# Optimization experiments

Measured on AMD Instinct MI355X. Metric: run time of the kernel, lower is better.

The kernel has to match this reference:

```python
import jax, jax.numpy as jnp
import numpy as np
from jax import lax


def _conv(x, w, b, pad, dil):
    # standard NCHW conv, OIHW weights
    y = lax.conv_general_dilated(x, w, (1, 1), [(pad, pad), (pad, pad)],
                                 rhs_dilation=(dil, dil),
                                 dimension_numbers=('NCHW', 'OIHW', 'NCHW'))
    return y + b[None, :, None, None]


def _bilinear(img, py, px):
    # img: [B,C,H,W]; py,px: [B,KK,H,W] float sample positions.
    # Zero-padding bilinear sampling (torchvision deform_conv semantics):
    # each of the 4 corners contributes 0 if it lies outside the image.
    B, C, H, W = img.shape
    y0 = jnp.floor(py)
    x0 = jnp.floor(px)
    wy1 = py - y0
    wx1 = px - x0
    imgf = img.reshape(B, C, H * W)

    def corner(yi, xi, wgt):
        valid = (yi >= 0) & (yi <= H - 1) & (xi >= 0) & (xi <= W - 1)
        yc = jnp.clip(yi, 0, H - 1).astype(jnp.int32)
        xc = jnp.clip(xi, 0, W - 1).astype(jnp.int32)
        idx = yc * W + xc  # [B,KK,H,W]
        g = jax.vmap(lambda im, ix: jnp.take(im, ix.reshape(-1), axis=1))(imgf, idx)
        g = g.reshape(B, C, *yi.shape[1:])  # [B,C,KK,H,W]
        return g * (wgt * valid.astype(img.dtype))[:, None]

    return (corner(y0, x0, (1 - wy1) * (1 - wx1))
            + corner(y0, x0 + 1, (1 - wy1) * wx1)
            + corner(y0 + 1, x0, wy1 * (1 - wx1))
            + corner(y0 + 1, x0 + 1, wy1 * wx1))


def _deform_dw(x, off_w, off_b, dw_w, K, pad, dil):
    # offset-predicted deformable depthwise conv (groups == channels)
    B, C, H, W = x.shape
    off = _conv(x, off_w, off_b, pad, dil).reshape(B, K * K, 2, H, W)
    dy, dx = off[:, :, 0], off[:, :, 1]  # torchvision order: (dy, dx) per tap
    ky, kx = jnp.meshgrid(jnp.arange(K), jnp.arange(K), indexing='ij')
    by = (ky.reshape(-1) * dil - pad).astype(x.dtype)  # [KK]
    bx = (kx.reshape(-1) * dil - pad).astype(x.dtype)
    py = jnp.arange(H, dtype=x.dtype)[None, None, :, None] + by[None, :, None, None] + dy
    px = jnp.arange(W, dtype=x.dtype)[None, None, None, :] + bx[None, :, None, None] + dx
    s = _bilinear(x, py, px)  # [B,C,KK,H,W]
    return jnp.einsum('bckhw,ck->bchw', s, dw_w.reshape(C, K * K))


def setup_inputs() -> dict:
    key = jax.random.key(0)
    ks = jax.random.split(key, 9)
    B, C, H, W = 4, 64, 56, 56
    f = lambda k, shape, s: jax.random.normal(k, shape, jnp.float32) * s
    return dict(
        x=f(ks[0], (B, C, H, W), 1.0),
        off_w1=f(ks[1], (2 * 5 * 5, C, 5, 5), 0.01), off_b1=f(ks[2], (2 * 5 * 5,), 0.01),
        dw_w1=f(ks[3], (C, 1, 5, 5), 0.1),
        off_w2=f(ks[4], (2 * 7 * 7, C, 7, 7), 0.01), off_b2=f(ks[5], (2 * 7 * 7,), 0.01),
        dw_w2=f(ks[6], (C, 1, 7, 7), 0.1),
        pw_w=f(ks[7], (C, C, 1, 1), 0.05), pw_b=f(ks[8], (C,), 0.05),
    )


def reference(x, off_w1, off_b1, dw_w1, off_w2, off_b2, dw_w2, pw_w, pw_b):
    attn = _deform_dw(x, off_w1, off_b1, dw_w1, 5, 2, 1)       # 5x5 deformable dw
    attn = _deform_dw(attn, off_w2, off_b2, dw_w2, 7, 9, 3)    # 7x7 dil-3 deformable dw
    attn = _conv(attn, pw_w, pw_b, 0, 1)                       # 1x1 pointwise
    return x * attn                                            # gated multiply
```

## Files before the change

kernel.cpp:

```cpp
#include <hip/hip_runtime.h>

#define BB 4
#define CC 64
#define HH 56
#define WW 56
#define HW (HH*WW)

typedef unsigned short u16;
typedef unsigned int u32;
typedef __attribute__((ext_vector_type(8))) short bf16x8;
typedef __attribute__((ext_vector_type(4))) float f32x4;

__device__ __forceinline__ u16 f2bf(float f) {
    union { float f; unsigned u; } c; c.f = f;
    unsigned u = c.u;
    u = (u + 0x7FFFu + ((u >> 16) & 1u)) >> 16;
    return (u16)u;
}
__device__ __forceinline__ float lo_f(u32 u) {
    union { unsigned u; float f; } c; c.u = u << 16; return c.f;
}
__device__ __forceinline__ float hi_f(u32 u) {
    union { unsigned u; float f; } c; c.u = u & 0xffff0000u; return c.f;
}

typedef const __attribute__((address_space(1))) unsigned int guint;
typedef __attribute__((address_space(3))) unsigned int luint;
__device__ __forceinline__ void gl_lds16(const void* g, void* l) {
    __builtin_amdgcn_global_load_lds((guint*)g, (luint*)l, 16, 0, 0);
}

#define W1P 60
#define PB1 3600
#define W2P 74
#define PB2 5476

#define R1 102400
#define R2 401408
#define R3 4096
#define R4 1600
#define R5 3136
#define R6z (BB*PB1*8)
#define R7z (BB*PB2*8)
#define TGRID (BB*(HW/64))
#define PREPN (R1+R2+R3+R4+R5+R6z+R7z)
__global__ __launch_bounds__(256)
void prep_tr_kernel(const float* __restrict__ x,
                    const float* __restrict__ ow1, const float* __restrict__ ow2,
                    const float* __restrict__ pw,  const float* __restrict__ dw1,
                    const float* __restrict__ dw2,
                    u16* __restrict__ xTp, u16* __restrict__ a1Tp,
                    u16* __restrict__ w2t1, u16* __restrict__ w2t2,
                    u16* __restrict__ pwT, float* __restrict__ dwT1,
                    float* __restrict__ dwT2) {
    __shared__ u16 tile[64][72];
    const int t = threadIdx.x;
    if (blockIdx.x < TGRID) {
        const int blk = blockIdx.x;
        const int b   = blk / (HW/64);
        const int p0  = (blk % (HW/64))*64;
        const int px  = t & 63, icq = t >> 6;
        const float* ip = x + ((size_t)b*CC + icq*16)*HW + p0 + px;
        #pragma unroll
        for (int i = 0; i < 16; ++i)
            tile[px][icq*16 + i] = f2bf(ip[(size_t)i*HW]);
        __syncthreads();
        const int px2 = t >> 2, g = t & 3;
        const int p = p0 + px2;
        const int y = p / WW, xw = p % WW;
        u16* op = xTp + ((size_t)b*PB1 + (y+2)*W1P + (xw+2))*64 + g*16;
        const uint4* s = (const uint4*)&tile[px2][g*16];
        ((uint4*)op)[0] = s[0];
        ((uint4*)op)[1] = s[1];
        return;
    }
    const int i = (blockIdx.x - TGRID)*256 + t;
    if (i < R1) {
        const int ic = i & 63, n = (i >> 6) & 63, tap = i >> 12;
        w2t1[i] = f2bf((n < 50) ? ow1[((size_t)n*64 + ic)*25 + tap] : 0.f);
    } else if (i < R1+R2) {
        const int j = i - R1;
        const int ic = j & 63, n = (j >> 6) & 127, tap = j >> 13;
        w2t2[j] = f2bf((n < 98) ? ow2[((size_t)n*64 + ic)*49 + tap] : 0.f);
    } else if (i < R1+R2+R3) {
        const int j = i - (R1+R2);
        pwT[j] = f2bf(pw[j]);
    } else if (i < R1+R2+R3+R4) {
        const int j = i - (R1+R2+R3);
        const int c = j & 63, k = j >> 6;
        dwT1[j] = dw1[c*25 + k];
    } else if (i < R1+R2+R3+R4+R5) {
        const int j = i - (R1+R2+R3+R4);
        const int c = j & 63, k = j >> 6;
        dwT2[j] = dw2[c*49 + k];
    } else if (i < R1+R2+R3+R4+R5+R6z) {
        const int j = i - (R1+R2+R3+R4+R5);
        const int c8 = j & 7, q = j >> 3;
        const int px = q % PB1, bz = q / PB1;
        const int y = px / W1P, xx = px % W1P;
        if (y < 2 || y >= 58 || xx < 2 || xx >= 58)
            *(uint4*)(xTp + ((size_t)bz*PB1 + px)*64 + c8*8) = make_uint4(0,0,0,0);
    } else if (i < PREPN) {
        const int j = i - (R1+R2+R3+R4+R5+R6z);
        const int c8 = j & 7, q = j >> 3;
        const int px = q % PB2, bz = q / PB2;
        const int y = px / W2P, xx = px % W2P;
        if (y < 9 || y >= 65 || xx < 9 || xx >= 65)
            *(uint4*)(a1Tp + ((size_t)bz*PB2 + px)*64 + c8*8) = make_uint4(0,0,0,0);
    }
}

template<int K, int DIL, int PAD, int COUT, int NP, int NPAD, int NTW>
__global__ __launch_bounds__(256, 4)
void conv_mfma_lds_kernel(const u16* __restrict__ xTp, const u16* __restrict__ w2t,
                          const float* __restrict__ bias, float* __restrict__ out) {
    constexpr int KK = K*K;
    constexpr int BROWS = 16*NTW;
    constexpr int WP  = WW + 2*PAD;
    constexpr int IPB = (HH + 2*PAD)*WP;
    __shared__ u16 Ab[2][64*64];
    __shared__ u16 Bb[2][BROWS*64];

    const int nm   = HW/64;
    const int b    = blockIdx.x / nm;
    const int p0   = (blockIdx.x % nm)*64;
    const int nt0  = blockIdx.y;
    const int t    = threadIdx.x;
    const int wave = t >> 6;
    const int lane = t & 63;

    const int spx = t >> 3;
    const int sc  = t & 7;
    const int gk8 = ((sc - spx) & 7)*8;
    const int pA  = p0 + spx;
    const int pB  = pA + 32;
    const int pyA = pA / WW, pxA = pA % WW;
    const int pyB = pB / WW, pxB = pB % WW;
    const u16* xb  = xTp + (size_t)b*IPB*64;
    const u16* gA0 = xb + ((size_t)((pyA+PAD)*WP + (pxA+PAD)))*64 + gk8;
    const u16* gA1 = xb + ((size_t)((pyB+PAD)*WP + (pxB+PAD)))*64 + gk8;
    const u16* gB  = w2t + (size_t)nt0*BROWS*64 + spx*64 + gk8;

    const int r = lane & 15, quad = lane >> 4;
    const int mloc = wave*16 + r;
    const int arow = mloc*64;
    const int a0s = ((quad     + mloc) & 7)*8;
    const int a1s = ((quad + 4 + mloc) & 7)*8;
    const int b0s = ((quad     + r) & 7)*8;
    const int b1s = ((quad + 4 + r) & 7)*8;

    f32x4 acc[NTW];
    #pragma unroll
    for (int h = 0; h < NTW; ++h) acc[h] = (f32x4){0.f,0.f,0.f,0.f};

    auto ISSUE = [&](int tap, int buf) {
        const int dyy = (tap/K)*DIL - PAD;
        const int dxx = (tap%K)*DIL - PAD;
        const int toff = (dyy*WP + dxx)*64;
        gl_lds16(gA0 + toff,           &Ab[buf][wave*512]);
        gl_lds16(gA1 + toff,           &Ab[buf][2048 + wave*512]);
        gl_lds16(gB + tap*(NP*64),     &Bb[buf][wave*512]);
    };

    ISSUE(0, 0);
    __syncthreads();

    #pragma unroll
    for (int tap = 0; tap < KK; ++tap) {
        if (tap + 1 < KK) ISSUE(tap + 1, (tap + 1) & 1);

        const u16* A  = &Ab[tap & 1][0];
        const u16* Bq = &Bb[tap & 1][0];
        const bf16x8 av0 = *(const bf16x8*)(A + arow + a0s);
        const bf16x8 av1 = *(const bf16x8*)(A + arow + a1s);
        #pragma unroll
        for (int h = 0; h < NTW; ++h) {
            const int brow = (h*16 + r)*64;
            const bf16x8 bv0 = *(const bf16x8*)(Bq + brow + b0s);
            const bf16x8 bv1 = *(const bf16x8*)(Bq + brow + b1s);
            acc[h] = __builtin_amdgcn_mfma_f32_16x16x32_bf16(av0, bv0, acc[h], 0, 0, 0);
            acc[h] = __builtin_amdgcn_mfma_f32_16x16x32_bf16(av1, bv1, acc[h], 0, 0, 0);
        }
        __syncthreads();
    }

    #pragma unroll
    for (int h = 0; h < NTW; ++h) {
        const int n = nt0*BROWS + h*16 + r;
        if (n < COUT) {
            const float bv = bias[n];
            float* op = out + ((size_t)b*HW + p0 + wave*16 + quad*4)*NPAD + n;
            #pragma unroll
            for (int r2 = 0; r2 < 4; ++r2) op[(size_t)r2*NPAD] = acc[h][r2] + bv;
        }
    }
}

template<int K, int DIL, int PAD, int NPAD,
         int IP, int IWP, int IPB, int OP, int OWP, int OPB>
__global__ __launch_bounds__(256)
void deform_cl_kernel(const u16* __restrict__ inT, const float* __restrict__ offT,
                      const float* __restrict__ dwT, u16* __restrict__ outT) {
    constexpr int KK = K*K;
    __shared__ float4 swt[8][KK];
    __shared__ int4   sat[8][KK];
    __shared__ float  sdw[KK*64];

    const int t = threadIdx.x;
    const int nb8 = (BB*HW/8) >> 3;
    const int blk0 = blockIdx.x;
    const int blk = (blk0 & 7)*nb8 + (blk0 >> 3);
    const int p0 = blk*8;
    const int b  = p0 / HW;
    const int pl0 = p0 - b*HW;

    for (int i = t; i < KK*64; i += 256) sdw[i] = dwT[i];

    for (int i = t; i < 8*KK; i += 256) {
        const int pix = i / KK, k = i - pix*KK;
        const int pl  = pl0 + pix;
        const int h = pl / WW, w = pl % WW;
        const float* orow = offT + ((size_t)b*HW + pl)*NPAD;
        const float dy = orow[2*k];
        const float dx = orow[2*k+1];
        const float py = (float)(h + (k/K)*DIL - PAD) + dy;
        const float px = (float)(w + (k%K)*DIL - PAD) + dx;
        const float y0f = floorf(py), x0f = floorf(px);
        const float wy1 = py - y0f,  wx1 = px - x0f;
        const float wy0 = 1.f - wy1, wx0 = 1.f - wx1;
        const int y0 = (int)y0f, x0 = (int)x0f;

        const int y0c = min(max(y0,   0), HH-1);
        const int y1c = min(max(y0+1, 0), HH-1);
        const int x0c = min(max(x0,   0), WW-1);
        const int x1c = min(max(x0+1, 0), WW-1);
        const float gy0 = wy0 * ((y0   >= 0 && y0   < HH) ? 1.f : 0.f);
        const float gy1 = wy1 * ((y0+1 >= 0 && y0+1 < HH) ? 1.f : 0.f);
        const float gx0 = wx0 * ((x0   >= 0 && x0   < WW) ? 1.f : 0.f);
        const float gx1 = wx1 * ((x0+1 >= 0 && x0+1 < WW) ? 1.f : 0.f);

        swt[pix][k] = make_float4(gy0*gx0, gy0*gx1, gy1*gx0, gy1*gx1);
        const int r0 = (y0c + IP)*IWP, r1 = (y1c + IP)*IWP;
        sat[pix][k] = make_int4((r0 + x0c + IP) << 7, (r0 + x1c + IP) << 7,
                                (r1 + x0c + IP) << 7, (r1 + x1c + IP) << 7);
    }
    __syncthreads();

    const int wave = t >> 6, lane = t & 63;
    const int pixl = 2*wave + (lane >> 5);
    const int chp  = lane & 31;
    const char* ib = (const char*)(inT + (size_t)b*IPB*64) + chp*4;

    float accx = 0.f, accy = 0.f;

    int4   av[3];
    float4 wv[2];
    float2 dv[2];
    u32 c00[2], c01[2], c10[2], c11[2];

    av[0] = sat[pixl][0];
    if (KK > 1) av[1] = sat[pixl][1];
    wv[0] = swt[pixl][0];
    dv[0] = *(const float2*)&sdw[2*chp];
    c00[0] = *(const u32*)(ib + av[0].x);
    c01[0] = *(const u32*)(ib + av[0].y);
    c10[0] = *(const u32*)(ib + av[0].z);
    c11[0] = *(const u32*)(ib + av[0].w);

    #pragma unroll
    for (int k = 0; k < KK; ++k) {
        const int kn = k + 1;
        if (kn + 1 < KK) av[(kn+1)%3] = sat[pixl][kn+1];
        if (kn < KK) {
            wv[kn&1] = swt[pixl][kn];
            dv[kn&1] = *(const float2*)&sdw[kn*64 + 2*chp];
            const int4 a = av[kn%3];
            c00[kn&1] = *(const u32*)(ib + a.x);
            c01[kn&1] = *(const u32*)(ib + a.y);
            c10[kn&1] = *(const u32*)(ib + a.z);
            c11[kn&1] = *(const u32*)(ib + a.w);
        }
        const float4 w = wv[k&1];
        const u32 u00 = c00[k&1], u01 = c01[k&1], u10 = c10[k&1], u11 = c11[k&1];
        const float sx = lo_f(u00)*w.x + lo_f(u01)*w.y + lo_f(u10)*w.z + lo_f(u11)*w.w;
        const float sy = hi_f(u00)*w.x + hi_f(u01)*w.y + hi_f(u10)*w.z + hi_f(u11)*w.w;
        const float2 d = dv[k&1];
        accx += sx * d.x;
        accy += sy * d.y;
    }

    const int oy = (pl0 + pixl) / WW, ox = (pl0 + pixl) % WW;
    const int opx = (oy + OP)*OWP + (ox + OP);
    const u32 o = (u32)f2bf(accx) | ((u32)f2bf(accy) << 16);
    *(u32*)((char*)outT + ((size_t)b*OPB + opx)*128 + chp*4) = o;
}

__global__ __launch_bounds__(256)
void pw_mfma_kernel(const u16* __restrict__ a2T, const u16* __restrict__ pwT,
                    const float* __restrict__ pb, const float* __restrict__ x,
                    float* __restrict__ out) {
    const int nm = HW/64;
    const int b  = blockIdx.x / nm;
    const int p0 = (blockIdx.x % nm)*64 + (threadIdx.x >> 6)*16;
    const int nt = blockIdx.y;
    const int lane = threadIdx.x & 63;
    const int r = lane & 15, quad = lane >> 4;

    const u16* ap = a2T + ((size_t)b*HW + p0 + r)*64 + quad*8;
    f32x4 acc = (f32x4){0.f,0.f,0.f,0.f};
    #pragma unroll
    for (int ks = 0; ks < 2; ++ks) {
        const bf16x8 av = *(const bf16x8*)(ap + ks*32);
        const bf16x8 bv = *(const bf16x8*)(pwT + ((size_t)(nt*16 + r))*64 + ks*32 + quad*8);
        acc = __builtin_amdgcn_mfma_f32_16x16x32_bf16(av, bv, acc, 0, 0, 0);
    }

    const int n = nt*16 + r;
    const float bv = pb[n];
    const size_t base = ((size_t)b*CC + n)*HW + p0 + quad*4;
    #pragma unroll
    for (int r2 = 0; r2 < 4; ++r2)
        out[base + r2] = x[base + r2] * (acc[r2] + bv);
}

template<int K, int DIL, int PAD, int COUT, int OCB>
__global__ __launch_bounds__(256)
void off_conv_sg_kernel(const float* __restrict__ in, const float* __restrict__ wgt,
                        const float* __restrict__ bias, float* __restrict__ out) {
    constexpr int KK = K*K;
    const int nOB = COUT / OCB;
    const int b   = blockIdx.x / nOB;
    const int oc0 = (blockIdx.x % nOB) * OCB;
    const int x   = threadIdx.x;
    const int h   = blockIdx.y*4 + threadIdx.y;

    float acc[OCB];
    #pragma unroll
    for (int o = 0; o < OCB; ++o) acc[o] = bias[oc0+o];

    const float* inb = in + (size_t)b*CC*HW;
    const float* wb  = wgt + (size_t)oc0*CC*KK;

    for (int ic = 0; ic < CC; ++ic) {
        const float* inp = inb + ic*HW;
        const float* wp  = wb + ic*KK;
        #pragma unroll
        for (int ky = 0; ky < K; ++ky) {
            const int  y  = h + ky*DIL - PAD;
            const bool yv = (y >= 0) && (y < HH);
            const int  yc = yv ? y : 0;
            const float* row = inp + yc*WW;
            #pragma unroll
            for (int kx = 0; kx < K; ++kx) {
                const int  xx = x + kx*DIL - PAD;
                const bool v  = yv && (xx >= 0) && (xx < WW);
                const int  xc = (xx < 0) ? 0 : ((xx >= WW) ? (WW-1) : xx);
                float val = row[xc];
                val = v ? val : 0.f;
                const int t = ky*K + kx;
                #pragma unroll
                for (int o = 0; o < OCB; ++o)
                    acc[o] += wp[(size_t)o*CC*KK + t] * val;
            }
        }
    }

    if (x >= WW) return;
    #pragma unroll
    for (int o = 0; o < OCB; ++o)
        out[((size_t)b*COUT + oc0 + o)*HW + h*WW + x] = acc[o];
}

template<int K, int DIL, int PAD>
__global__ __launch_bounds__(64)
void deform_dw_full_kernel(const float* __restrict__ in, const float* __restrict__ off,
                           const float* __restrict__ dw, float* __restrict__ out) {
    constexpr int KK = K*K;
    const int idx = blockIdx.x*64 + threadIdx.x;
    const int x = idx % WW;
    const int h = (idx / WW) % HH;
    const int c = (idx / HW) % CC;
    const int b = idx / (CC*HW);

    const float* inp  = in  + ((size_t)b*CC + c)*HW;
    const float* offp = off + (size_t)b*(2*KK)*HW + h*WW + x;
    const float* dwp  = dw  + c*KK;

    float acc = 0.f;
    #pragma unroll 7
    for (int k = 0; k < KK; ++k) {
        const float dy = offp[(2*k  )*HW];
        const float dx = offp[(2*k+1)*HW];
        const float py = (float)(h + (k/K)*DIL - PAD) + dy;
        const float px = (float)(x + (k%K)*DIL - PAD) + dx;
        const float y0f = floorf(py), x0f = floorf(px);
        const float wy1 = py - y0f,  wx1 = px - x0f;
        const float wy0 = 1.f - wy1, wx0 = 1.f - wx1;
        const int y0 = (int)y0f, x0 = (int)x0f;

        const int y0c = min(max(y0,   0), HH-1);
        const int y1c = min(max(y0+1, 0), HH-1);
        const int x0c = min(max(x0,   0), WW-1);
        const int x1c = min(max(x0+1, 0), WW-1);
        const float my0 = (y0   >= 0 && y0   < HH) ? 1.f : 0.f;
        const float my1 = (y0+1 >= 0 && y0+1 < HH) ? 1.f : 0.f;
        const float mx0 = (x0   >= 0 && x0   < WW) ? 1.f : 0.f;
        const float mx1 = (x0+1 >= 0 && x0+1 < WW) ? 1.f : 0.f;

        const float v00 = inp[y0c*WW + x0c];
        const float v01 = inp[y0c*WW + x1c];
        const float v10 = inp[y1c*WW + x0c];
        const float v11 = inp[y1c*WW + x1c];

        const float gx0 = wx0*mx0, gx1 = wx1*mx1;
        const float s = (v00*gx0 + v01*gx1) * (wy0*my0)
                      + (v10*gx0 + v11*gx1) * (wy1*my1);
        acc += s * dwp[k];
    }
    out[idx] = acc;
}

__global__ __launch_bounds__(256)
void pw_mul_kernel(const float* __restrict__ x, const float* __restrict__ a2,
                   const float* __restrict__ pw, const float* __restrict__ pb,
                   float* __restrict__ out) {
    constexpr int HW4 = HW/4;
    const int t = blockIdx.x*256 + threadIdx.x;
    if (t >= BB*CC*HW4) return;
    const int sp4 = t % HW4;
    const int oc  = (t / HW4) % CC;
    const int b   = t / (CC*HW4);

    const float4* ap = (const float4*)(a2 + (size_t)b*CC*HW) + sp4;
    const float4* wp4 = (const float4*)(pw + oc*CC);
    const float pbv = pb[oc];
    float4 acc = make_float4(pbv, pbv, pbv, pbv);
    #pragma unroll 4
    for (int ic4 = 0; ic4 < CC/4; ++ic4) {
        const float4 w = wp4[ic4];
        float4 a0 = ap[(ic4*4+0)*HW4];
        float4 a1 = ap[(ic4*4+1)*HW4];
        float4 a2v = ap[(ic4*4+2)*HW4];
        float4 a3 = ap[(ic4*4+3)*HW4];
        acc.x += w.x*a0.x + w.y*a1.x + w.z*a2v.x + w.w*a3.x;
        acc.y += w.x*a0.y + w.y*a1.y + w.z*a2v.y + w.w*a3.y;
        acc.z += w.x*a0.z + w.y*a1.z + w.z*a2v.z + w.w*a3.z;
        acc.w += w.x*a0.w + w.y*a1.w + w.z*a2v.w + w.w*a3.w;
    }
    const float4 xv = ((const float4*)x)[t];
    float4 r;
    r.x = xv.x*acc.x; r.y = xv.y*acc.y; r.z = xv.z*acc.z; r.w = xv.w*acc.w;
    ((float4*)out)[t] = r;
}

extern "C" void kernel_launch(void* const* d_in, const int* in_sizes, int n_in,
                              void* d_out, int out_size, void* d_ws, size_t ws_size,
                              hipStream_t stream) {
    const float* x      = (const float*)d_in[0];
    const float* off_w1 = (const float*)d_in[1];
    const float* off_b1 = (const float*)d_in[2];
    const float* dw_w1  = (const float*)d_in[3];
    const float* off_w2 = (const float*)d_in[4];
    const float* off_b2 = (const float*)d_in[5];
    const float* dw_w2  = (const float*)d_in[6];
    const float* pw_w   = (const float*)d_in[7];
    const float* pw_b   = (const float*)d_in[8];
    float* out = (float*)d_out;

    const size_t nF    = (size_t)BB*CC*HW;
    const size_t attnB = nF*sizeof(float);
    const size_t off2B = (size_t)BB*98*HW*sizeof(float);
    const size_t offTB = (size_t)BB*HW*112*sizeof(float);
    const size_t chB   = (size_t)BB*HW*64*sizeof(u16);
    const size_t xpB   = (size_t)BB*PB1*64*sizeof(u16);
    const size_t a1pB  = (size_t)BB*PB2*64*sizeof(u16);
    char* ws = (char*)d_ws;

    const int n    = (int)nF;
    const int dbl  = n/64;
    const int pbl  = (n/4 + 255)/256;
    dim3 cblk(64,4);
    dim3 rgrd1(BB*(50/5), HH/4);
    dim3 rgrd2(BB*(98/7), HH/4);
    dim3 cgrd1(TGRID, 2);
    dim3 cgrd2(TGRID, 4);
    dim3 pgrd(TGRID, 4);
    const int dgrid = BB*HW/8;

    const size_t oOFF  = 0;
    const size_t oXTP  = oOFF  + offTB;
    const size_t oA1TP = oXTP  + xpB;
    const size_t oA2T  = oA1TP + a1pB;
    const size_t oW1   = oA2T  + chB;
    const size_t oW2   = oW1   + (size_t)R1*2;
    const size_t oPWT  = oW2   + (size_t)R2*2;
    const size_t oDW1  = oPWT  + (size_t)R3*2;
    const size_t oDW2  = oDW1  + (size_t)R4*4;
    const size_t TOT   = oDW2  + (size_t)R5*4;

    if (ws_size >= TOT) {
        float* off_buf = (float*)(ws + oOFF);
        u16*   xTp     = (u16*)(ws + oXTP);
        u16*   a1Tp    = (u16*)(ws + oA1TP);
        u16*   a2T     = (u16*)(ws + oA2T);
        u16*   w2t1    = (u16*)(ws + oW1);
        u16*   w2t2    = (u16*)(ws + oW2);
        u16*   pwT     = (u16*)(ws + oPWT);
        float* dwT1    = (float*)(ws + oDW1);
        float* dwT2    = (float*)(ws + oDW2);

        prep_tr_kernel<<<TGRID + (PREPN+255)/256, 256, 0, stream>>>(
            x, off_w1, off_w2, pw_w, dw_w1, dw_w2,
            xTp, a1Tp, w2t1, w2t2, pwT, dwT1, dwT2);

        conv_mfma_lds_kernel<5,1,2,50,64,64,2><<<cgrd1, 256, 0, stream>>>(xTp, w2t1, off_b1, off_buf);
        deform_cl_kernel<5,1,2,64, 2,W1P,PB1, 9,W2P,PB2><<<dgrid, 256, 0, stream>>>(xTp, off_buf, dwT1, a1Tp);

        conv_mfma_lds_kernel<7,3,9,98,128,112,2><<<cgrd2, 256, 0, stream>>>(a1Tp, w2t2, off_b2, off_buf);
        deform_cl_kernel<7,3,9,112, 9,W2P,PB2, 0,WW,HW><<<dgrid, 256, 0, stream>>>(a1Tp, off_buf, dwT2, a2T);

        pw_mfma_kernel<<<pgrd, 256, 0, stream>>>(a2T, pwT, pw_b, x, out);
    } else if (ws_size >= off2B + attnB) {
        float* off_buf = (float*)ws;
        float* attn1   = (float*)d_out;
        float* attn2   = (float*)(ws + off2B);
        off_conv_sg_kernel<5,1,2,50,5><<<rgrd1, cblk, 0, stream>>>(x, off_w1, off_b1, off_buf);
        deform_dw_full_kernel<5,1,2><<<dbl, 64, 0, stream>>>(x, off_buf, dw_w1, attn1);
        off_conv_sg_kernel<7,3,9,98,7><<<rgrd2, cblk, 0, stream>>>(attn1, off_w2, off_b2, off_buf);
        deform_dw_full_kernel<7,3,9><<<dbl, 64, 0, stream>>>(attn1, off_buf, dw_w2, attn2);
        pw_mul_kernel<<<pbl, 256, 0, stream>>>(x, attn2, pw_w, pw_b, out);
    } else {
        float* attn1 = (float*)d_out;
        float* attn2 = (float*)ws;
        float* off1  = (float*)ws;
        off_conv_sg_kernel<5,1,2,50,5><<<rgrd1, cblk, 0, stream>>>(x, off_w1, off_b1, off1);
        deform_dw_full_kernel<5,1,2><<<dbl, 64, 0, stream>>>(x, off1, dw_w1, attn1);
        float* off2 = (float*)(ws + attnB);
        off_conv_sg_kernel<7,3,9,98,7><<<rgrd2, cblk, 0, stream>>>(attn1, off_w2, off_b2, off2);
        deform_dw_full_kernel<7,3,9><<<dbl, 64, 0, stream>>>(attn1, off2, dw_w2, attn2);
        pw_mul_kernel<<<pbl, 256, 0, stream>>>(x, attn2, pw_w, pw_b, out);
    }
}
```

Baseline: 162.1 us.

## Load conv A operands directly from global and stage weights per kernel row

The offset-predicting convolution kernels stop staging the activation tile through LDS. Each lane now reads its bf16x8 A fragments straight from the padded channels-last global buffer, and only the weight tiles, one full kernel row of taps at a time, are double-buffered into LDS. The weight layout is pre-swizzled in the prep kernel so the LDS reads stay bank-conflict free. Each block now covers 16 output channels instead of 32, which doubles the grid's y dimension (more blocks, less reuse of A per block). Barriers drop from one per tap to one per kernel row, but global A loads now sit directly in the MFMA dependency chain without an LDS prefetch.

Result: slower. 214.0 us (+32.0%).

```diff
diff --git a/kernel.cpp b/kernel.cpp
--- a/kernel.cpp
+++ b/kernel.cpp
@@ -77,11 +77,13 @@
     const int i = (blockIdx.x - TGRID)*256 + t;
     if (i < R1) {
         const int ic = i & 63, n = (i >> 6) & 63, tap = i >> 12;
-        w2t1[i] = f2bf((n < 50) ? ow1[((size_t)n*64 + ic)*25 + tap] : 0.f);
+        const int sw = ((((ic >> 3) + n) & 7) << 3) | (ic & 7);
+        w2t1[(i & ~63) | sw] = f2bf((n < 50) ? ow1[((size_t)n*64 + ic)*25 + tap] : 0.f);
     } else if (i < R1+R2) {
         const int j = i - R1;
         const int ic = j & 63, n = (j >> 6) & 127, tap = j >> 13;
-        w2t2[j] = f2bf((n < 98) ? ow2[((size_t)n*64 + ic)*49 + tap] : 0.f);
+        const int sw = ((((ic >> 3) + n) & 7) << 3) | (ic & 7);
+        w2t2[(j & ~63) | sw] = f2bf((n < 98) ? ow2[((size_t)n*64 + ic)*49 + tap] : 0.f);
     } else if (i < R1+R2+R3) {
         const int j = i - (R1+R2);
         pwT[j] = f2bf(pw[j]);
@@ -110,16 +112,12 @@
     }
 }
 
-template<int K, int DIL, int PAD, int COUT, int NP, int NPAD, int NTW>
+template<int K, int DIL, int PAD, int COUT, int NP, int NPAD>
 __global__ __launch_bounds__(256, 4)
-void conv_mfma_lds_kernel(const u16* __restrict__ xTp, const u16* __restrict__ w2t,
-                          const float* __restrict__ bias, float* __restrict__ out) {
-    constexpr int KK = K*K;
-    constexpr int BROWS = 16*NTW;
-    constexpr int WP  = WW + 2*PAD;
-    constexpr int IPB = (HH + 2*PAD)*WP;
-    __shared__ u16 Ab[2][64*64];
-    __shared__ u16 Bb[2][BROWS*64];
+void conv_mfma_ad_kernel(const u16* __restrict__ inTp, const u16* __restrict__ w2t,
+                         const float* __restrict__ bias, float* __restrict__ out) {
+    constexpr int WP = WW + 2*PAD;
+    __shared__ u16 Bb[2][K*16*64];
 
     const int nm   = HW/64;
     const int b    = blockIdx.x / nm;
@@ -128,71 +126,55 @@
     const int t    = threadIdx.x;
     const int wave = t >> 6;
     const int lane = t & 63;
-
-    const int spx = t >> 3;
-    const int sc  = t & 7;
-    const int gk8 = ((sc - spx) & 7)*8;
-    const int pA  = p0 + spx;
-    const int pB  = pA + 32;
-    const int pyA = pA / WW, pxA = pA % WW;
-    const int pyB = pB / WW, pxB = pB % WW;
-    const u16* xb  = xTp + (size_t)b*IPB*64;
-    const u16* gA0 = xb + ((size_t)((pyA+PAD)*WP + (pxA+PAD)))*64 + gk8;
-    const u16* gA1 = xb + ((size_t)((pyB+PAD)*WP + (pxB+PAD)))*64 + gk8;
-    const u16* gB  = w2t + (size_t)nt0*BROWS*64 + spx*64 + gk8;
-
     const int r = lane & 15, quad = lane >> 4;
-    const int mloc = wave*16 + r;
-    const int arow = mloc*64;
-    const int a0s = ((quad     + mloc) & 7)*8;
-    const int a1s = ((quad + 4 + mloc) & 7)*8;
+
+    const int mpx = p0 + wave*16 + r;
+    const int py = mpx / WW, px = mpx % WW;
+    const u16* aptr = inTp + ((size_t)b*((HH+2*PAD)*WP) + (size_t)(py+PAD)*WP + (px+PAD))*64 + quad*8;
+
+    const u16* wsrc = w2t + (size_t)nt0*16*64 + lane*8;
+
     const int b0s = ((quad     + r) & 7)*8;
     const int b1s = ((quad + 4 + r) & 7)*8;
 
-    f32x4 acc[NTW];
-    #pragma unroll
-    for (int h = 0; h < NTW; ++h) acc[h] = (f32x4){0.f,0.f,0.f,0.f};
-
-    auto ISSUE = [&](int tap, int buf) {
-        const int dyy = (tap/K)*DIL - PAD;
-        const int dxx = (tap%K)*DIL - PAD;
-        const int toff = (dyy*WP + dxx)*64;
-        gl_lds16(gA0 + toff,           &Ab[buf][wave*512]);
-        gl_lds16(gA1 + toff,           &Ab[buf][2048 + wave*512]);
-        gl_lds16(gB + tap*(NP*64),     &Bb[buf][wave*512]);
+    f32x4 acc = (f32x4){0.f,0.f,0.f,0.f};
+
+    auto STAGE = [&](int c) {
+        u16* dst = &Bb[c & 1][0];
+        for (int s = wave; s < 2*K; s += 4) {
+            const int tap = c*K + (s >> 1);
+            gl_lds16(wsrc + (size_t)tap*NP*64 + (s & 1)*512,
+                     dst + (s >> 1)*1024 + (s & 1)*512);
+        }
     };
 
-    ISSUE(0, 0);
+    STAGE(0);
     __syncthreads();
 
-    #pragma unroll
-    for (int tap = 0; tap < KK; ++tap) {
-        if (tap + 1 < KK) ISSUE(tap + 1, (tap + 1) & 1);
-
-        const u16* A  = &Ab[tap & 1][0];
-        const u16* Bq = &Bb[tap & 1][0];
-        const bf16x8 av0 = *(const bf16x8*)(A + arow + a0s);
-        const bf16x8 av1 = *(const bf16x8*)(A + arow + a1s);
+    for (int c = 0; c < K; ++c) {
+        if (c + 1 < K) STAGE(c + 1);
+        const u16* Bq = &Bb[c & 1][0];
+        const int arow0 = (c*DIL - PAD)*WP*64;
         #pragma unroll
-        for (int h = 0; h < NTW; ++h) {
-            const int brow = (h*16 + r)*64;
-            const bf16x8 bv0 = *(const bf16x8*)(Bq + brow + b0s);
-            const bf16x8 bv1 = *(const bf16x8*)(Bq + brow + b1s);
-            acc[h] = __builtin_amdgcn_mfma_f32_16x16x32_bf16(av0, bv0, acc[h], 0, 0, 0);
-            acc[h] = __builtin_amdgcn_mfma_f32_16x16x32_bf16(av1, bv1, acc[h], 0, 0, 0);
+        for (int kk = 0; kk < K; ++kk) {
+            const int aoff = arow0 + (kk*DIL - PAD)*64;
+            const bf16x8 av0 = *(const bf16x8*)(aptr + aoff);
+            const bf16x8 av1 = *(const bf16x8*)(aptr + aoff + 32);
+            const u16* Brow = Bq + kk*1024 + r*64;
+            const bf16x8 bv0 = *(const bf16x8*)(Brow + b0s);
+            const bf16x8 bv1 = *(const bf16x8*)(Brow + b1s);
+            acc = __builtin_amdgcn_mfma_f32_16x16x32_bf16(av0, bv0, acc, 0, 0, 0);
+            acc = __builtin_amdgcn_mfma_f32_16x16x32_bf16(av1, bv1, acc, 0, 0, 0);
         }
         __syncthreads();
     }
 
-    #pragma unroll
-    for (int h = 0; h < NTW; ++h) {
-        const int n = nt0*BROWS + h*16 + r;
-        if (n < COUT) {
-            const float bv = bias[n];
-            float* op = out + ((size_t)b*HW + p0 + wave*16 + quad*4)*NPAD + n;
-            #pragma unroll
-            for (int r2 = 0; r2 < 4; ++r2) op[(size_t)r2*NPAD] = acc[h][r2] + bv;
-        }
+    const int n = nt0*16 + r;
+    if (n < COUT) {
+        const float bv = bias[n];
+        float* op = out + ((size_t)b*HW + p0 + wave*16 + quad*4)*NPAD + n;
+        #pragma unroll
+        for (int r2 = 0; r2 < 4; ++r2) op[(size_t)r2*NPAD] = acc[r2] + bv;
     }
 }
 
@@ -482,8 +464,8 @@
     dim3 cblk(64,4);
     dim3 rgrd1(BB*(50/5), HH/4);
     dim3 rgrd2(BB*(98/7), HH/4);
-    dim3 cgrd1(TGRID, 2);
-    dim3 cgrd2(TGRID, 4);
+    dim3 cgrd1(TGRID, 4);
+    dim3 cgrd2(TGRID, 7);
     dim3 pgrd(TGRID, 4);
     const int dgrid = BB*HW/8;
 
@@ -513,10 +495,10 @@
             x, off_w1, off_w2, pw_w, dw_w1, dw_w2,
             xTp, a1Tp, w2t1, w2t2, pwT, dwT1, dwT2);
 
-        conv_mfma_lds_kernel<5,1,2,50,64,64,2><<<cgrd1, 256, 0, stream>>>(xTp, w2t1, off_b1, off_buf);
+        conv_mfma_ad_kernel<5,1,2,50,64,64><<<cgrd1, 256, 0, stream>>>(xTp, w2t1, off_b1, off_buf);
         deform_cl_kernel<5,1,2,64, 2,W1P,PB1, 9,W2P,PB2><<<dgrid, 256, 0, stream>>>(xTp, off_buf, dwT1, a1Tp);
 
-        conv_mfma_lds_kernel<7,3,9,98,128,112,2><<<cgrd2, 256, 0, stream>>>(a1Tp, w2t2, off_b2, off_buf);
+        conv_mfma_ad_kernel<7,3,9,98,128,112><<<cgrd2, 256, 0, stream>>>(a1Tp, w2t2, off_b2, off_buf);
         deform_cl_kernel<7,3,9,112, 9,W2P,PB2, 0,WW,HW><<<dgrid, 256, 0, stream>>>(a1Tp, off_buf, dwT2, a2T);
 
         pw_mfma_kernel<<<pgrd, 256, 0, stream>>>(a2T, pwT, pw_b, x, out);
```
